# Kernel optimization log

Hardware: AMD Instinct MI355X
Metric: run time of the kernel (lower is better)

Reference implementation:

```python
import jax, jax.numpy as jnp
import numpy as np


def setup_inputs() -> dict:
    key = jax.random.key(0)
    kq, kk, kv, km = jax.random.split(key, 4)
    B, H, S, D = 2, 8, 4096, 64
    queries = jax.random.normal(kq, (B, H, S, D), dtype=jnp.float32)
    keys = jax.random.normal(kk, (B, H, S, D), dtype=jnp.float32)
    values = jax.random.normal(kv, (B, H, S, D), dtype=jnp.float32)
    mask = jax.random.randint(km, (1, 1, S, S), 0, 2).astype(jnp.bool_)
    return {"queries": queries, "keys": keys, "values": values, "d_k": D, "mask": mask}


def reference(queries, keys, values, d_k, mask):
    # scores: [B, H, S, S]
    scale = 1.0 / jnp.sqrt(jnp.float32(d_k))
    scores = jnp.einsum("bhqd,bhkd->bhqk", queries, keys) * scale
    scores = jnp.where(mask, scores, jnp.float32(-1e9))  # masked_fill(~mask, -1e9)
    weights = jax.nn.softmax(scores, axis=-1)
    # non-standard post-softmax clip: min(|mask_as_float|, |weights|)
    weights = jnp.minimum(jnp.abs(mask.astype(jnp.float32)), jnp.abs(weights))
    return jnp.einsum("bhqk,bhkd->bhqd", weights, values)
```

## Files before the change

kernel.cpp:

```cpp
#include <hip/hip_runtime.h>
#include <stdint.h>

#define S_LEN 4096
#define SCALE_LOG2E 0.18033688011112042f

typedef __attribute__((ext_vector_type(8))) short bf16x8;
typedef __attribute__((ext_vector_type(4))) float f32x4;

#if __has_builtin(__builtin_amdgcn_exp2f)
#define EXP2(x) __builtin_amdgcn_exp2f(x)
#else
#define EXP2(x) exp2f(x)
#endif

#if __has_builtin(__builtin_amdgcn_sbfe)
#define SBFE1(x, o) __builtin_amdgcn_sbfe((int)(x), (o), 1)
#else
#define SBFE1(x, o) (((int)((unsigned)(x) << (31 - (o)))) >> 31)
#endif

__device__ __forceinline__ unsigned pk2(float a, float b) {
    unsigned ua = __builtin_bit_cast(unsigned, a) + 0x8000u;
    unsigned ub = __builtin_bit_cast(unsigned, b) + 0x8000u;
    return __builtin_amdgcn_perm(ub, ua, 0x07060302u);
}

__device__ __forceinline__ unsigned cvtpk(float a, float b) {
    unsigned r;
    asm("v_cvt_pk_bf16_f32 %0, %1, %2" : "=v"(r) : "v"(a), "v"(b));
    return r;
}

__device__ __forceinline__ f32x4 mfma16(bf16x8 a, bf16x8 b, f32x4 c) {
    return __builtin_amdgcn_mfma_f32_16x16x32_bf16(a, b, c, 0, 0, 0);
}

__device__ __forceinline__ bf16x8 bf16_ones() {
    uint4 q = {0x3F803F80u, 0x3F803F80u, 0x3F803F80u, 0x3F803F80u};
    return __builtin_bit_cast(bf16x8, q);
}

__device__ __forceinline__ void gld16(const void* g, void* l) {
    __builtin_amdgcn_global_load_lds(
        (const __attribute__((address_space(1))) unsigned*)g,
        (__attribute__((address_space(3))) unsigned*)l, 16, 0, 0);
}

__device__ __forceinline__ unsigned long long spread4_16(unsigned long long x) {
    x = (x | (x << 24)) & 0x000000FF000000FFull;
    x = (x | (x << 12)) & 0x000F000F000F000Full;
    x = (x | (x << 6))  & 0x0303030303030303ull;
    x = (x | (x << 3))  & 0x1111111111111111ull;
    return x;
}

__device__ __forceinline__ void pack_mask_body(
    const unsigned* __restrict__ m32, unsigned long long* __restrict__ out,
    int lane, int w, bool is_word) {
    const unsigned char* m8 = (const unsigned char*)m32;
    for (int bx = blockIdx.x; bx < 16384; bx += gridDim.x) {
        const long long W0 = (long long)bx * 16 + w * 4;
        const long long q = W0 >> 6;
        const long long kt0 = W0 & 63;
        unsigned long long bal[4];
        if (is_word) {
            const uint4 v = *(const uint4*)(m32 + (W0 * 64 + 4 * lane));
            bal[0] = __ballot(v.x != 0u);
            bal[1] = __ballot(v.y != 0u);
            bal[2] = __ballot(v.z != 0u);
            bal[3] = __ballot(v.w != 0u);
        } else {
            const unsigned v = *(const unsigned*)(m8 + (W0 * 64 + 4 * lane));
            bal[0] = __ballot((v & 0x000000FFu) != 0u);
            bal[1] = __ballot((v & 0x0000FF00u) != 0u);
            bal[2] = __ballot((v & 0x00FF0000u) != 0u);
            bal[3] = __ballot((v & 0xFF000000u) != 0u);
        }
        if (lane == 0) {
#pragma unroll
            for (int wd = 0; wd < 4; ++wd) {
                unsigned long long ow =
                    spread4_16((bal[0] >> (16 * wd)) & 0xFFFFull) |
                    (spread4_16((bal[1] >> (16 * wd)) & 0xFFFFull) << 1) |
                    (spread4_16((bal[2] >> (16 * wd)) & 0xFFFFull) << 2) |
                    (spread4_16((bal[3] >> (16 * wd)) & 0xFFFFull) << 3);
                out[(kt0 + wd) * S_LEN + q] = ow;
            }
        }
    }
}

__device__ __forceinline__ bool mask_is_word_mode(const unsigned* __restrict__ m32,
                                                  int lane) {
    unsigned pv = m32[lane];
    bool okw = (pv == 0u) || (pv == 1u) || (pv == 0x3F800000u);
    return (__ballot(okw) == ~0ull);
}

__device__ __forceinline__ void pf_load(const float* __restrict__ K,
                                        const float* __restrict__ V,
                                        int bh, int k0, int t,
                                        unsigned* kb, unsigned* vb) {
    const int r = t >> 2, h = t & 3;
    const float* kp = K + (((size_t)(bh * S_LEN + k0 + r)) << 6) + h * 16;
#pragma unroll
    for (int cc = 0; cc < 2; ++cc) {
        float4 f0 = ((const float4*)kp)[cc * 2];
        float4 f1 = ((const float4*)kp)[cc * 2 + 1];
        kb[cc * 4 + 0] = pk2(f0.x, f0.y);
        kb[cc * 4 + 1] = pk2(f0.z, f0.w);
        kb[cc * 4 + 2] = pk2(f1.x, f1.y);
        kb[cc * 4 + 3] = pk2(f1.z, f1.w);
    }
    const int d = t & 63, g = t >> 6;
    const float* vp = V + (((size_t)(bh * S_LEN + k0 + g * 16)) << 6) + d;
#pragma unroll
    for (int c8 = 0; c8 < 2; ++c8) {
        float f[8];
#pragma unroll
        for (int i = 0; i < 8; ++i) f[i] = vp[(c8 * 8 + i) * 64];
        vb[c8 * 4 + 0] = pk2(f[0], f[1]);
        vb[c8 * 4 + 1] = pk2(f[2], f[3]);
        vb[c8 * 4 + 2] = pk2(f[4], f[5]);
        vb[c8 * 4 + 3] = pk2(f[6], f[7]);
    }
}

__device__ __forceinline__ void pf_store(int t, const unsigned* kb, const unsigned* vb,
                                         unsigned short* lk, unsigned short* lv) {
    const int r = t >> 2, h = t & 3;
#pragma unroll
    for (int cc = 0; cc < 2; ++cc) {
        int c = h * 2 + cc;
        uint4 st = {kb[cc * 4 + 0], kb[cc * 4 + 1], kb[cc * 4 + 2], kb[cc * 4 + 3]};
        *(uint4*)&lk[r * 64 + ((c ^ (r & 7)) << 3)] = st;
    }
    const int d = t & 63, g = t >> 6;
#pragma unroll
    for (int c8 = 0; c8 < 2; ++c8) {
        int c = g * 2 + c8;
        uint4 st = {vb[c8 * 4 + 0], vb[c8 * 4 + 1], vb[c8 * 4 + 2], vb[c8 * 4 + 3]};
        *(uint4*)&lv[d * 64 + ((c ^ (d & 7)) << 3)] = st;
    }
}

__global__ __launch_bounds__(256) void prep_kernel(
    const unsigned* __restrict__ m32, unsigned long long* __restrict__ out,
    const float* __restrict__ K, const float* __restrict__ V,
    unsigned short* __restrict__ kv) {
    const int t = threadIdx.x;
    if (blockIdx.x < 1024) {
        const int kt = blockIdx.x & 63;
        const int bh = blockIdx.x >> 6;
        unsigned kb[8], vb[8];
        pf_load(K, V, bh, kt * 64, t, kb, vb);
        unsigned short* base = kv + ((size_t)(bh * 64 + kt)) * 8192;
        pf_store(t, kb, vb, base, base + 4096);
    }
    const int lane = t & 63;
    const int w = t >> 6;
    const bool is_word = mask_is_word_mode(m32, lane);
    pack_mask_body(m32, out, lane, w, is_word);
}

__global__ __launch_bounds__(256) void pack_mask_kernel(
    const unsigned* __restrict__ m32, unsigned long long* __restrict__ out) {
    const int lane = threadIdx.x & 63;
    const int w = threadIdx.x >> 6;
    const bool is_word = mask_is_word_mode(m32, lane);
    pack_mask_body(m32, out, lane, w, is_word);
}

__device__ __forceinline__ void stage_tile8(const unsigned short* kvtile,
                                            unsigned short* lk, unsigned short* lv,
                                            int tid) {
    const int w = tid >> 6;
    const int lane = tid & 63;
    const char* g = (const char*)kvtile + w * 1024 + lane * 16;
    gld16(g, (char*)lk + w * 1024);
    gld16(g + 8192, (char*)lv + w * 1024);
}

template <int USE_PACKED>
__device__ __forceinline__ void compute_tile(
    int kt, int q0w, int n16, int quad,
    const unsigned long long (&mrow)[2],
    const unsigned* __restrict__ rawmask, int mask_is_word,
    const unsigned short* lk, const unsigned short* lv, unsigned short* lp,
    const bf16x8 (&aq)[2][2], f32x4 (&oacc)[4][2], f32x4 (&oaccl)[2]) {
    const int k0 = kt * 64;
    const f32x4 z = {0.f, 0.f, 0.f, 0.f};
    unsigned nmw[2][2];
    if (USE_PACKED) {
#pragma unroll
        for (int nt = 0; nt < 2; ++nt) {
            unsigned long long nm = ~(mrow[nt] >> (quad * 4));
            nmw[nt][0] = (unsigned)nm;
            nmw[nt][1] = (unsigned)(nm >> 32);
        }
    }
#pragma unroll
    for (int mth = 0; mth < 2; ++mth) {
        f32x4 sac[2][2];
#pragma unroll
        for (int mi = 0; mi < 2; ++mi)
#pragma unroll
            for (int nt = 0; nt < 2; ++nt) {
                if (USE_PACKED) {
                    const int mt = mth * 2 + mi;
#pragma unroll
                    for (int reg = 0; reg < 4; ++reg) {
                        unsigned ext = (unsigned)SBFE1(nmw[nt][mt >> 1], (mt & 1) * 16 + reg);
                        sac[mi][nt][reg] = __builtin_bit_cast(float, 0xFF800000u & ext);
                    }
                } else {
                    sac[mi][nt] = z;
                }
            }
        __builtin_amdgcn_s_setprio(1);
#pragma unroll
        for (int kd = 0; kd < 2; ++kd) {
#pragma unroll
            for (int mi = 0; mi < 2; ++mi) {
                int row = (mth * 2 + mi) * 16 + n16;
                bf16x8 ak = *(const bf16x8*)&lk[row * 64 + (((kd * 4 + quad) ^ (row & 7)) << 3)];
#pragma unroll
                for (int nt = 0; nt < 2; ++nt)
                    sac[mi][nt] = mfma16(ak, aq[nt][kd], sac[mi][nt]);
            }
        }
        __builtin_amdgcn_s_setprio(0);
#pragma unroll
        for (int mi = 0; mi < 2; ++mi) {
#pragma unroll
            for (int nt = 0; nt < 2; ++nt) {
                const int mt = mth * 2 + mi;
                float p[4];
#pragma unroll
                for (int reg = 0; reg < 4; ++reg) {
                    float e = EXP2(sac[mi][nt][reg]);
                    if (!USE_PACKED) {
                        int pos = mt * 16 + quad * 4 + reg;
                        size_t mi2 = (size_t)(q0w + nt * 16 + n16) * S_LEN + k0 + pos;
                        bool bit = mask_is_word ? (rawmask[mi2] != 0u)
                                                : (((const unsigned char*)rawmask)[mi2] != 0);
                        e = bit ? e : 0.0f;
                    }
                    p[reg] = e;
                }
                uint2 pr = {cvtpk(p[0], p[1]), cvtpk(p[2], p[3])};
                const int r = nt * 16 + n16;
                const int chunk = (mt * 2 + (quad >> 1)) ^ (n16 & 7);
                *(uint2*)((char*)lp + r * 128 + chunk * 16 + (quad & 1) * 8) = pr;
            }
        }
    }
    const bf16x8 onesv = bf16_ones();
    __builtin_amdgcn_s_setprio(1);
#pragma unroll
    for (int kk = 0; kk < 2; ++kk) {
        bf16x8 av[4];
#pragma unroll
        for (int md = 0; md < 4; ++md) {
            int dr = md * 16 + n16;
            av[md] = *(const bf16x8*)&lv[dr * 64 + (((kk * 4 + quad) ^ (dr & 7)) << 3)];
        }
#pragma unroll
        for (int nt = 0; nt < 2; ++nt) {
            const int r = nt * 16 + n16;
            const int chunk = (kk * 4 + quad) ^ (n16 & 7);
            bf16x8 pb = *(const bf16x8*)((const char*)lp + r * 128 + chunk * 16);
#pragma unroll
            for (int md = 0; md < 4; ++md)
                oacc[md][nt] = mfma16(av[md], pb, oacc[md][nt]);
            oaccl[nt] = mfma16(onesv, pb, oaccl[nt]);
        }
    }
    __builtin_amdgcn_s_setprio(0);
}

__device__ __forceinline__ void load_q_frags(const float* __restrict__ Q, int bh, int q0w,
                                             int n16, int quad, bf16x8 (&aq)[2][2]) {
#pragma unroll
    for (int nt = 0; nt < 2; ++nt) {
        const float* qp = Q + ((size_t)(bh * S_LEN + q0w + nt * 16 + n16) << 6);
#pragma unroll
        for (int kd = 0; kd < 2; ++kd) {
            float4 f0 = *(const float4*)(qp + kd * 32 + quad * 8);
            float4 f1 = *(const float4*)(qp + kd * 32 + quad * 8 + 4);
            uint4 u = {pk2(f0.x * SCALE_LOG2E, f0.y * SCALE_LOG2E),
                       pk2(f0.z * SCALE_LOG2E, f0.w * SCALE_LOG2E),
                       pk2(f1.x * SCALE_LOG2E, f1.y * SCALE_LOG2E),
                       pk2(f1.z * SCALE_LOG2E, f1.w * SCALE_LOG2E)};
            aq[nt][kd] = __builtin_bit_cast(bf16x8, u);
        }
    }
}

__global__ __launch_bounds__(512, 4) void attn_partial2(
    const float* __restrict__ Q, const unsigned short* __restrict__ KV,
    const unsigned long long* __restrict__ pm,
    float* __restrict__ Opart, float* __restrict__ Lpart) {
    __shared__ __align__(16) unsigned short lk[2][64 * 64];
    __shared__ __align__(16) unsigned short lv[2][64 * 64];
    __shared__ __align__(16) unsigned short lpbuf[8][32 * 64];
    const int tid = threadIdx.x;
    const int lane = tid & 63;
    const int w = tid >> 6;
    const int n16 = lane & 15;
    const int quad = lane >> 4;
    const int bh = blockIdx.y;
    const int half = blockIdx.z;
    const int q0w = blockIdx.x * 256 + w * 32;
    unsigned short* lp = lpbuf[w];
    const unsigned short* kvb = KV + (size_t)bh * (64 * 8192) + (size_t)(half * 32) * 8192;

    bf16x8 aq[2][2];
    load_q_frags(Q, bh, q0w, n16, quad, aq);

    f32x4 oacc[4][2];
    f32x4 oaccl[2];
    const f32x4 z = {0.f, 0.f, 0.f, 0.f};
#pragma unroll
    for (int md = 0; md < 4; ++md)
#pragma unroll
        for (int nt = 0; nt < 2; ++nt) oacc[md][nt] = z;
    oaccl[0] = z;
    oaccl[1] = z;

    stage_tile8(kvb, lk[0], lv[0], tid);
    unsigned long long mrow_cur[2], mrow_nxt[2];
#pragma unroll
    for (int nt = 0; nt < 2; ++nt)
        mrow_cur[nt] = pm[(size_t)(half * 32) * S_LEN + q0w + nt * 16 + n16];

    for (int ktl = 0; ktl < 32; ++ktl) {
        const int cur = ktl & 1;
        const int ktn = (ktl + 1) & 31;
        __syncthreads();
        stage_tile8(kvb + (size_t)ktn * 8192,
                    cur ? lk[0] : lk[1], cur ? lv[0] : lv[1], tid);
#pragma unroll
        for (int nt = 0; nt < 2; ++nt)
            mrow_nxt[nt] = pm[(size_t)(half * 32 + ktn) * S_LEN + q0w + nt * 16 + n16];
        compute_tile<1>(half * 32 + ktl, q0w, n16, quad, mrow_cur, nullptr, 1,
                        cur ? lk[1] : lk[0], cur ? lv[1] : lv[0], lp, aq, oacc, oaccl);
        mrow_cur[0] = mrow_nxt[0];
        mrow_cur[1] = mrow_nxt[1];
    }

#pragma unroll
    for (int nt = 0; nt < 2; ++nt) {
        int q = q0w + nt * 16 + n16;
        if (quad == 0) Lpart[((size_t)(half * 16 + bh) << 12) + q] = oaccl[nt][0];
#pragma unroll
        for (int md = 0; md < 4; ++md) {
            float4 o;
            o.x = oacc[md][nt][0];
            o.y = oacc[md][nt][1];
            o.z = oacc[md][nt][2];
            o.w = oacc[md][nt][3];
            *(float4*)(Opart + (((size_t)(half * 16 + bh) << 12) + q) * 64 +
                       md * 16 + quad * 4) = o;
        }
    }
}

__global__ __launch_bounds__(256, 3) void attn_partial(
    const float* __restrict__ Q, const float* __restrict__ K, const float* __restrict__ V,
    const unsigned long long* __restrict__ pm,
    float* __restrict__ Opart, float* __restrict__ Lpart) {
    __shared__ __align__(16) unsigned short lk[2][64 * 64];
    __shared__ __align__(16) unsigned short lv[2][64 * 64];
    __shared__ __align__(16) unsigned short lpbuf[4][32 * 64];
    const int tid = threadIdx.x;
    const int lane = tid & 63;
    const int w = tid >> 6;
    const int n16 = lane & 15;
    const int quad = lane >> 4;
    const int bh = blockIdx.y;
    const int half = blockIdx.z;
    const int q0w = blockIdx.x * 128 + w * 32;
    const int kbase = half * 2048;
    unsigned short* lp = lpbuf[w];

    bf16x8 aq[2][2];
    load_q_frags(Q, bh, q0w, n16, quad, aq);

    f32x4 oacc[4][2];
    f32x4 oaccl[2];
    const f32x4 z = {0.f, 0.f, 0.f, 0.f};
#pragma unroll
    for (int md = 0; md < 4; ++md)
#pragma unroll
        for (int nt = 0; nt < 2; ++nt) oacc[md][nt] = z;
    oaccl[0] = z;
    oaccl[1] = z;

    unsigned kb[8], vb[8];
    pf_load(K, V, bh, kbase, tid, kb, vb);
    pf_store(tid, kb, vb, lk[0], lv[0]);
    unsigned long long mrow_cur[2], mrow_nxt[2];
#pragma unroll
    for (int nt = 0; nt < 2; ++nt)
        mrow_cur[nt] = pm[(size_t)(half * 32) * S_LEN + q0w + nt * 16 + n16];

    for (int ktl = 0; ktl < 32; ++ktl) {
        const int cur = ktl & 1;
        const int ktn = (ktl + 1) & 31;
        __syncthreads();
        pf_load(K, V, bh, kbase + ktn * 64, tid, kb, vb);
#pragma unroll
        for (int nt = 0; nt < 2; ++nt)
            mrow_nxt[nt] = pm[(size_t)(half * 32 + ktn) * S_LEN + q0w + nt * 16 + n16];
        compute_tile<1>(half * 32 + ktl, q0w, n16, quad, mrow_cur, nullptr, 1,
                        cur ? lk[1] : lk[0], cur ? lv[1] : lv[0], lp, aq, oacc, oaccl);
        pf_store(tid, kb, vb, cur ? lk[0] : lk[1], cur ? lv[0] : lv[1]);
        mrow_cur[0] = mrow_nxt[0];
        mrow_cur[1] = mrow_nxt[1];
    }

#pragma unroll
    for (int nt = 0; nt < 2; ++nt) {
        int q = q0w + nt * 16 + n16;
        if (quad == 0) Lpart[((size_t)(half * 16 + bh) << 12) + q] = oaccl[nt][0];
#pragma unroll
        for (int md = 0; md < 4; ++md) {
            float4 o;
            o.x = oacc[md][nt][0];
            o.y = oacc[md][nt][1];
            o.z = oacc[md][nt][2];
            o.w = oacc[md][nt][3];
            *(float4*)(Opart + (((size_t)(half * 16 + bh) << 12) + q) * 64 +
                       md * 16 + quad * 4) = o;
        }
    }
}

__global__ __launch_bounds__(256) void combine_kernel(
    const float* __restrict__ Opart, const float* __restrict__ Lpart,
    float* __restrict__ O) {
    for (int bx = blockIdx.x; bx < 16 * S_LEN / 16; bx += gridDim.x) {
        const int row = bx * 16 + (threadIdx.x >> 4);
        const int d4 = (threadIdx.x & 15) * 4;
        const float* p0 = Opart + (size_t)row * 64 + d4;
        const float* p1 = p0 + (size_t)16 * S_LEN * 64;
        float4 a = *(const float4*)p0;
        float4 b = *(const float4*)p1;
        float l = Lpart[row] + Lpart[16 * S_LEN + row];
        float r = (l > 0.f) ? (1.0f / l) : 0.0f;
        float4 o;
        o.x = (a.x + b.x) * r;
        o.y = (a.y + b.y) * r;
        o.z = (a.z + b.z) * r;
        o.w = (a.w + b.w) * r;
        *(float4*)(O + (size_t)row * 64 + d4) = o;
    }
}

template <int USE_PACKED>
__global__ __launch_bounds__(256, 3) void attn_kernel(
    const float* __restrict__ Q, const float* __restrict__ K, const float* __restrict__ V,
    const unsigned long long* __restrict__ pm, const unsigned* __restrict__ rawmask,
    float* __restrict__ O) {
    __shared__ __align__(16) unsigned short lk[2][64 * 64];
    __shared__ __align__(16) unsigned short lv[2][64 * 64];
    __shared__ __align__(16) unsigned short lpbuf[4][32 * 64];
    const int tid = threadIdx.x;
    const int lane = tid & 63;
    const int w = tid >> 6;
    const int n16 = lane & 15;
    const int quad = lane >> 4;
    const int bh = blockIdx.y;
    const int q0w = blockIdx.x * 128 + w * 32;
    unsigned short* lp = lpbuf[w];

    int mask_is_word = 1;
    if (!USE_PACKED) {
        unsigned v = rawmask[lane];
        bool okw = (v == 0u) || (v == 1u) || (v == 0x3F800000u);
        mask_is_word = (__ballot(okw) == ~0ull) ? 1 : 0;
    }

    bf16x8 aq[2][2];
    load_q_frags(Q, bh, q0w, n16, quad, aq);

    f32x4 oacc[4][2];
    f32x4 oaccl[2];
    const f32x4 z = {0.f, 0.f, 0.f, 0.f};
#pragma unroll
    for (int md = 0; md < 4; ++md)
#pragma unroll
        for (int nt = 0; nt < 2; ++nt) oacc[md][nt] = z;
    oaccl[0] = z;
    oaccl[1] = z;

    unsigned kb[8], vb[8];
    pf_load(K, V, bh, 0, tid, kb, vb);
    pf_store(tid, kb, vb, lk[0], lv[0]);
    unsigned long long mrow_cur[2] = {0, 0}, mrow_nxt[2] = {0, 0};
    if (USE_PACKED) {
#pragma unroll
        for (int nt = 0; nt < 2; ++nt)
            mrow_cur[nt] = pm[(size_t)0 * S_LEN + q0w + nt * 16 + n16];
    }

    for (int kt = 0; kt < 64; ++kt) {
        const int cur = kt & 1;
        const int ktn = (kt + 1) & 63;
        __syncthreads();
        pf_load(K, V, bh, ktn * 64, tid, kb, vb);
        if (USE_PACKED) {
#pragma unroll
            for (int nt = 0; nt < 2; ++nt)
                mrow_nxt[nt] = pm[(size_t)ktn * S_LEN + q0w + nt * 16 + n16];
        }
        compute_tile<USE_PACKED>(kt, q0w, n16, quad, mrow_cur, rawmask, mask_is_word,
                                 cur ? lk[1] : lk[0], cur ? lv[1] : lv[0], lp, aq, oacc,
                                 oaccl);
        pf_store(tid, kb, vb, cur ? lk[0] : lk[1], cur ? lv[0] : lv[1]);
        mrow_cur[0] = mrow_nxt[0];
        mrow_cur[1] = mrow_nxt[1];
    }

    float rcpl[2];
#pragma unroll
    for (int nt = 0; nt < 2; ++nt) {
        float l = oaccl[nt][0];
        rcpl[nt] = (l > 0.f) ? (1.0f / l) : 0.0f;
    }
#pragma unroll
    for (int md = 0; md < 4; ++md)
#pragma unroll
        for (int nt = 0; nt < 2; ++nt) {
            int q = q0w + nt * 16 + n16;
            float4 o;
            o.x = oacc[md][nt][0] * rcpl[nt];
            o.y = oacc[md][nt][1] * rcpl[nt];
            o.z = oacc[md][nt][2] * rcpl[nt];
            o.w = oacc[md][nt][3] * rcpl[nt];
            *(float4*)(O + ((size_t)(bh * S_LEN + q) << 6) + md * 16 + quad * 4) = o;
        }
}

extern "C" void kernel_launch(void* const* d_in, const int* in_sizes, int n_in,
                              void* d_out, int out_size, void* d_ws, size_t ws_size,
                              hipStream_t stream) {
    (void)in_sizes; (void)n_in; (void)out_size;
    const float* Q = (const float*)d_in[0];
    const float* K = (const float*)d_in[1];
    const float* V = (const float*)d_in[2];
    const void* mask = d_in[4];
    float* O = (float*)d_out;

    const size_t bitfield_bytes = (size_t)S_LEN * S_LEN / 8;
    const size_t opart_bytes = (size_t)2 * 16 * S_LEN * 64 * 4;
    const size_t lpart_bytes = (size_t)2 * 16 * S_LEN * 4;
    const size_t kv_bytes = (size_t)16 * S_LEN * 64 * 2 * 2;
    const size_t need_packed = 1024 + bitfield_bytes;
    const size_t need_split = need_packed + opart_bytes + lpart_bytes;
    const size_t need_full = need_split + kv_bytes;

    unsigned long long* pmw = (unsigned long long*)((char*)d_ws + 1024);
    float* opart = (float*)((char*)d_ws + need_packed);
    float* lpart = opart + (size_t)2 * 16 * S_LEN * 64;
    unsigned short* kvp = (unsigned short*)((char*)d_ws + need_split);

    if (d_ws != nullptr && ws_size >= need_full) {
        prep_kernel<<<dim3(2048), 256, 0, stream>>>(
            (const unsigned*)mask, pmw, K, V, kvp);
        attn_partial2<<<dim3(S_LEN / 256, 16, 2), 512, 0, stream>>>(
            Q, kvp, pmw, opart, lpart);
        combine_kernel<<<dim3(1024), 256, 0, stream>>>(opart, lpart, O);
    } else if (d_ws != nullptr && ws_size >= need_split) {
        pack_mask_kernel<<<dim3(2048), 256, 0, stream>>>((const unsigned*)mask, pmw);
        attn_partial<<<dim3(S_LEN / 128, 16, 2), 256, 0, stream>>>(
            Q, K, V, pmw, opart, lpart);
        combine_kernel<<<dim3(1024), 256, 0, stream>>>(opart, lpart, O);
    } else if (d_ws != nullptr && ws_size >= need_packed) {
        pack_mask_kernel<<<dim3(2048), 256, 0, stream>>>((const unsigned*)mask, pmw);
        attn_kernel<1><<<dim3(S_LEN / 128, 16), 256, 0, stream>>>(
            Q, K, V, pmw, (const unsigned*)mask, O);
    } else {
        attn_kernel<0><<<dim3(S_LEN / 128, 16), 256, 0, stream>>>(
            Q, K, V, nullptr, (const unsigned*)mask, O);
    }
}
```

Measured before the change: 244.5 us.

## Fuse split-KV combine into attention kernel via atomic last-block reduction

Result: slower. 359.3 us (+47.0%).

```diff
diff --git a/kernel.cpp b/kernel.cpp
--- a/kernel.cpp
+++ b/kernel.cpp
@@ -147,8 +147,9 @@
 __global__ __launch_bounds__(256) void prep_kernel(
     const unsigned* __restrict__ m32, unsigned long long* __restrict__ out,
     const float* __restrict__ K, const float* __restrict__ V,
-    unsigned short* __restrict__ kv) {
+    unsigned short* __restrict__ kv, int* __restrict__ cnt) {
     const int t = threadIdx.x;
+    if (blockIdx.x == 0) cnt[t] = 0;
     if (blockIdx.x < 1024) {
         const int kt = blockIdx.x & 63;
         const int bh = blockIdx.x >> 6;
@@ -300,10 +301,12 @@
 __global__ __launch_bounds__(512, 4) void attn_partial2(
     const float* __restrict__ Q, const unsigned short* __restrict__ KV,
     const unsigned long long* __restrict__ pm,
-    float* __restrict__ Opart, float* __restrict__ Lpart) {
+    float* __restrict__ Opart, float* __restrict__ Lpart,
+    float* __restrict__ O, int* __restrict__ cnt) {
     __shared__ __align__(16) unsigned short lk[2][64 * 64];
     __shared__ __align__(16) unsigned short lv[2][64 * 64];
     __shared__ __align__(16) unsigned short lpbuf[8][32 * 64];
+    __shared__ int second_flag;
     const int tid = threadIdx.x;
     const int lane = tid & 63;
     const int w = tid >> 6;
@@ -362,6 +365,31 @@
             o.w = oacc[md][nt][3];
             *(float4*)(Opart + (((size_t)(half * 16 + bh) << 12) + q) * 64 +
                        md * 16 + quad * 4) = o;
+        }
+    }
+
+    __builtin_amdgcn_fence(__ATOMIC_RELEASE, "agent");
+    if (tid == 0) second_flag = atomicAdd(cnt + (bh * 16 + blockIdx.x), 1);
+    __syncthreads();
+    if (second_flag == 1) {
+        __builtin_amdgcn_fence(__ATOMIC_ACQUIRE, "agent");
+        const int oh = half ^ 1;
+#pragma unroll
+        for (int nt = 0; nt < 2; ++nt) {
+            int q = q0w + nt * 16 + n16;
+            float l = oaccl[nt][0] + Lpart[((size_t)(oh * 16 + bh) << 12) + q];
+            float r = (l > 0.f) ? (1.0f / l) : 0.0f;
+#pragma unroll
+            for (int md = 0; md < 4; ++md) {
+                float4 b = *(const float4*)(Opart +
+                    (((size_t)(oh * 16 + bh) << 12) + q) * 64 + md * 16 + quad * 4);
+                float4 o;
+                o.x = (oacc[md][nt][0] + b.x) * r;
+                o.y = (oacc[md][nt][1] + b.y) * r;
+                o.z = (oacc[md][nt][2] + b.z) * r;
+                o.w = (oacc[md][nt][3] + b.w) * r;
+                *(float4*)(O + ((size_t)(bh * S_LEN + q) << 6) + md * 16 + quad * 4) = o;
+            }
         }
     }
 }
@@ -561,6 +589,7 @@
     const size_t need_split = need_packed + opart_bytes + lpart_bytes;
     const size_t need_full = need_split + kv_bytes;
 
+    int* cnt = (int*)d_ws;
     unsigned long long* pmw = (unsigned long long*)((char*)d_ws + 1024);
     float* opart = (float*)((char*)d_ws + need_packed);
     float* lpart = opart + (size_t)2 * 16 * S_LEN * 64;
@@ -568,10 +597,9 @@
 
     if (d_ws != nullptr && ws_size >= need_full) {
         prep_kernel<<<dim3(2048), 256, 0, stream>>>(
-            (const unsigned*)mask, pmw, K, V, kvp);
+            (const unsigned*)mask, pmw, K, V, kvp, cnt);
         attn_partial2<<<dim3(S_LEN / 256, 16, 2), 512, 0, stream>>>(
-            Q, kvp, pmw, opart, lpart);
-        combine_kernel<<<dim3(1024), 256, 0, stream>>>(opart, lpart, O);
+            Q, kvp, pmw, opart, lpart, O, cnt);
     } else if (d_ws != nullptr && ws_size >= need_split) {
         pack_mask_kernel<<<dim3(2048), 256, 0, stream>>>((const unsigned*)mask, pmw);
         attn_partial<<<dim3(S_LEN / 128, 16, 2), 256, 0, stream>>>(
```
